# Performance work log

Hardware: AMD Instinct MI355X
Metric: run time of the kernel (lower is better)

The kernel has to match this reference:

```python
import jax, jax.numpy as jnp
import numpy as np

N_TP = 4  # number of heterogeneous agent types (experts)


def _mlp(x, w1, b1, w2, b2, w3, b3):
    h = jax.nn.relu(x @ w1 + b1)
    h = jax.nn.relu(h @ w2 + b2)
    return h @ w3 + b3


def setup_inputs() -> dict:
    key = jax.random.key(0)
    ks = jax.random.split(key, 12)
    T, A, D, H, NA = 2048, 128, 64, 64, 16
    s = 0.05
    return {
        "obs": jax.random.normal(ks[0], (T, A, D), dtype=jnp.float32),
        "hete_pick": jax.random.randint(ks[1], (T, A), 0, N_TP, dtype=jnp.int64),
        "gp_sel_summary": jax.random.uniform(ks[2], (T, N_TP), dtype=jnp.float32),
        "W1": jax.random.normal(ks[3], (N_TP, D + N_TP, H), dtype=jnp.float32) * s,
        "b1": jnp.zeros((N_TP, H), jnp.float32),
        "W2": jax.random.normal(ks[4], (N_TP, H, H), dtype=jnp.float32) * s,
        "b2": jnp.zeros((N_TP, H), jnp.float32),
        "W3": jax.random.normal(ks[5], (N_TP, H, NA), dtype=jnp.float32) * s,
        "b3": jnp.zeros((N_TP, NA), jnp.float32),
        "cW1": jax.random.normal(ks[6], (D + N_TP, H), dtype=jnp.float32) * s,
        "cb1": jnp.zeros((H,), jnp.float32),
        "cW2": jax.random.normal(ks[7], (H, H), dtype=jnp.float32) * s,
        "cb2": jnp.zeros((H,), jnp.float32),
        "cW3": jax.random.normal(ks[8], (H, 1), dtype=jnp.float32) * s,
        "cb3": jnp.zeros((1,), jnp.float32),
    }


def reference(obs, hete_pick, gp_sel_summary, W1, b1, W2, b2, W3, b3,
              cW1, cb1, cW2, cb2, cW3, cb3):
    T, A, D = obs.shape
    n_tp = W1.shape[0]
    # hete_info_obs: broadcast group-selection summary over agents, concat to obs
    hete_info = jnp.broadcast_to(gp_sel_summary[:, None, :], (T, A, n_tp))
    x = jnp.concatenate([obs, hete_info.astype(obs.dtype)], axis=-1)  # [T,A,D+n_tp]
    xf = x.reshape(T * A, D + n_tp)
    tp = hete_pick.reshape(T * A)
    # per-type dispatch: mask -> sub-net -> scatter back (expressed as masked select)
    logits = jnp.zeros((T * A, W3.shape[-1]), obs.dtype)
    for t in range(n_tp):
        out_t = _mlp(xf, W1[t], b1[t], W2[t], b2[t], W3[t], b3[t])
        logits = jnp.where((tp == t)[:, None], out_t, logits)
    # central critic runs on all agents
    value = _mlp(xf, cW1, cb1, cW2, cb2, cW3, cb3)  # [T*A,1]
    out = jnp.concatenate([logits, value], axis=-1)  # [T*A, n_action+1]
    return out.reshape(T, A, -1)
```

## Files before the change

kernel.cpp:

```cpp
#include <hip/hip_runtime.h>
#include <stdint.h>


typedef float v4f __attribute__((ext_vector_type(4)));
typedef short v8s __attribute__((ext_vector_type(8)));

#define WP2_OFF 30720
#define WP3_OFF 51200

static __device__ __forceinline__ short f2bf(float f) {
    union { float f; uint32_t u; } c; c.f = f;
    uint32_t u = c.u;
    uint32_t r = (u + 0x7FFFu + ((u >> 16) & 1u)) >> 16;
    return (short)r;
}
static __device__ __forceinline__ uint32_t pk2(float a, float b) {
    return (uint32_t)(uint16_t)f2bf(a) | ((uint32_t)(uint16_t)f2bf(b) << 16);
}

__global__ void prep_kernel(const float* __restrict__ W1, const float* __restrict__ cW1,
                            const float* __restrict__ W2, const float* __restrict__ cW2,
                            const float* __restrict__ W3, const float* __restrict__ cW3,
                            short* __restrict__ wp) {
    int b = blockIdx.x, lane = threadIdx.x;
    int nl = lane & 15, quad = lane >> 4;
    short frag[8];
    if (b < 60) {
        int e = b / 12, rem = b % 12, ks = rem / 4, nt = rem % 4;
        int n = nt * 16 + nl;
#pragma unroll
        for (int j = 0; j < 8; j++) {
            int k = ks * 32 + quad * 8 + j;
            float v = 0.f;
            if (k < 68) v = (e < 4) ? W1[(e * 68 + k) * 64 + n] : cW1[k * 64 + n];
            frag[j] = f2bf(v);
        }
    } else if (b < 100) {
        int u = b - 60, e = u / 8, ks = (u % 8) / 4, nt = u % 4;
        int n = nt * 16 + nl;
#pragma unroll
        for (int j = 0; j < 8; j++) {
            int k = ks * 32 + quad * 8 + j;
            frag[j] = f2bf((e < 4) ? W2[(e * 64 + k) * 64 + n] : cW2[k * 64 + n]);
        }
    } else {
        int u = b - 100;
#pragma unroll
        for (int j = 0; j < 8; j++) {
            int ks = (u < 8) ? (u & 1) : (u - 8);
            int k  = ks * 32 + quad * 8 + j;
            float v;
            if (u < 8) { int ee = u >> 1; v = W3[(ee * 64 + k) * 16 + nl]; }
            else       { v = (nl == 0) ? cW3[k] : 0.f; }
            frag[j] = f2bf(v);
        }
    }
    v8s pk = { frag[0], frag[1], frag[2], frag[3], frag[4], frag[5], frag[6], frag[7] };
    *(v8s*)(wp + (size_t)b * 512 + lane * 8) = pk;
}


__global__ __launch_bounds__(256, 3) void main_kernel(
    const float* __restrict__ obs, const float* __restrict__ gp,
    const int* __restrict__ hete, const short* __restrict__ wp,
    const float* __restrict__ b1, const float* __restrict__ b2, const float* __restrict__ b3,
    const float* __restrict__ cb1, const float* __restrict__ cb2, const float* __restrict__ cb3,
    float* __restrict__ out)
{
    __shared__ __align__(16) uint32_t H_[4][64 * 36];
    int tid = threadIdx.x, wv = tid >> 6, lane = tid & 63;
    int ml = lane & 15, quad = lane >> 4;
    uint32_t* H = H_[wv];
    int base = (blockIdx.x * 4 + wv) * 64;

    v8s      xf[2][4];
    uint32_t gpk[4][2];
    int      tpv[4];
    float    oE[4][4];
    float    oV[4];

#pragma unroll
    for (int tt = 0; tt < 4; tt++) {
        int tok = base + tt * 16 + ml;
        tpv[tt] = hete[tok];
        const float* xr = obs + (size_t)tok * 64 + quad * 8;
#pragma unroll
        for (int ks = 0; ks < 2; ks++) {
            float4 a = *(const float4*)(xr + ks * 32);
            float4 c = *(const float4*)(xr + ks * 32 + 4);
            v8s f;
            f[0] = f2bf(a.x); f[1] = f2bf(a.y); f[2] = f2bf(a.z); f[3] = f2bf(a.w);
            f[4] = f2bf(c.x); f[5] = f2bf(c.y); f[6] = f2bf(c.z); f[7] = f2bf(c.w);
            xf[ks][tt] = f;
        }
        if (quad == 0) {
            float4 g = *(const float4*)(gp + (size_t)(tok >> 7) * 4);
            gpk[tt][0] = pk2(g.x, g.y); gpk[tt][1] = pk2(g.z, g.w);
        } else { gpk[tt][0] = 0; gpk[tt][1] = 0; }
    }

    float cb3v = cb3[0];

    for (int ne = 0; ne < 5; ne++) {
        v4f acc[4][4];
#pragma unroll
        for (int tt = 0; tt < 4; tt++)
#pragma unroll
            for (int nt = 0; nt < 4; nt++) acc[tt][nt] = (v4f){0.f, 0.f, 0.f, 0.f};
#pragma unroll
        for (int ks = 0; ks < 3; ks++) {
            v8s wa[4];
#pragma unroll
            for (int nt = 0; nt < 4; nt++)
                wa[nt] = *(const v8s*)(wp + (size_t)((ne * 3 + ks) * 4 + nt) * 512 + lane * 8);
#pragma unroll
            for (int tt = 0; tt < 4; tt++) {
                v8s xb;
                if (ks < 2) xb = xf[ks][tt];
                else {
                    union { uint32_t u[4]; v8s s; } cv;
                    cv.u[0] = gpk[tt][0]; cv.u[1] = gpk[tt][1]; cv.u[2] = 0; cv.u[3] = 0;
                    xb = cv.s;
                }
#pragma unroll
                for (int nt = 0; nt < 4; nt++)
                    acc[tt][nt] = __builtin_amdgcn_mfma_f32_16x16x32_bf16(wa[nt], xb, acc[tt][nt], 0, 0, 0);
            }
        }
        const float* B1 = (ne < 4) ? (b1 + ne * 64) : cb1;
        float4 bv[4];
#pragma unroll
        for (int nt = 0; nt < 4; nt++) bv[nt] = *(const float4*)(B1 + nt * 16 + quad * 4);
#pragma unroll
        for (int tt = 0; tt < 4; tt++) {
            int tL = tt * 16 + ml, rb = tL * 36, sw = tL & 7;
#pragma unroll
            for (int nt = 0; nt < 4; nt++) {
                float v0 = fmaxf(acc[tt][nt][0] + bv[nt].x, 0.f);
                float v1 = fmaxf(acc[tt][nt][1] + bv[nt].y, 0.f);
                float v2 = fmaxf(acc[tt][nt][2] + bv[nt].z, 0.f);
                float v3 = fmaxf(acc[tt][nt][3] + bv[nt].w, 0.f);
                int g = 2 * nt + (quad >> 1);
                uint2 w2 = { pk2(v0, v1), pk2(v2, v3) };
                *(uint2*)&H[rb + ((g ^ sw) << 2) + 2 * (quad & 1)] = w2;
            }
        }
        v8s wa2[2][4];
#pragma unroll
        for (int ks2 = 0; ks2 < 2; ks2++)
#pragma unroll
            for (int nt = 0; nt < 4; nt++)
                wa2[ks2][nt] = *(const v8s*)(wp + WP2_OFF +
                    (size_t)((ne * 2 + ks2) * 4 + nt) * 512 + lane * 8);
        const float* B2 = (ne < 4) ? (b2 + ne * 64) : cb2;
        float4 bv2[4];
#pragma unroll
        for (int nt = 0; nt < 4; nt++) bv2[nt] = *(const float4*)(B2 + nt * 16 + quad * 4);
        v8s w3f[2];
#pragma unroll
        for (int ks2 = 0; ks2 < 2; ks2++)
            w3f[ks2] = *(const v8s*)(wp + WP3_OFF +
                (size_t)((ne < 4) ? (ne * 2 + ks2) : (8 + ks2)) * 512 + lane * 8);
        float4 b3v = (ne < 4) ? *(const float4*)(b3 + ne * 16 + quad * 4)
                              : (float4){0.f, 0.f, 0.f, 0.f};

#pragma unroll
        for (int tt = 0; tt < 4; tt++) {
            int tL = tt * 16 + ml, rb = tL * 36, sw = tL & 7;
            v4f a2[4];
#pragma unroll
            for (int nt = 0; nt < 4; nt++) a2[nt] = (v4f){0.f, 0.f, 0.f, 0.f};
#pragma unroll
            for (int ks2 = 0; ks2 < 2; ks2++) {
                v8s hf = *(const v8s*)&H[rb + (((4 * ks2 + quad) ^ sw) << 2)];
#pragma unroll
                for (int nt = 0; nt < 4; nt++)
                    a2[nt] = __builtin_amdgcn_mfma_f32_16x16x32_bf16(wa2[ks2][nt], hf, a2[nt], 0, 0, 0);
            }
#pragma unroll
            for (int nt = 0; nt < 4; nt++) {
                float v0 = fmaxf(a2[nt][0] + bv2[nt].x, 0.f);
                float v1 = fmaxf(a2[nt][1] + bv2[nt].y, 0.f);
                float v2 = fmaxf(a2[nt][2] + bv2[nt].z, 0.f);
                float v3 = fmaxf(a2[nt][3] + bv2[nt].w, 0.f);
                int g = 2 * nt + (quad >> 1);
                uint2 w2 = { pk2(v0, v1), pk2(v2, v3) };
                *(uint2*)&H[rb + ((g ^ sw) << 2) + 2 * (quad & 1)] = w2;
            }
            v4f a3 = (v4f){0.f, 0.f, 0.f, 0.f};
#pragma unroll
            for (int ks2 = 0; ks2 < 2; ks2++) {
                v8s hf2 = *(const v8s*)&H[rb + (((4 * ks2 + quad) ^ sw) << 2)];
                a3 = __builtin_amdgcn_mfma_f32_16x16x32_bf16(w3f[ks2], hf2, a3, 0, 0, 0);
            }
            if (ne < 4) {
#pragma unroll
                for (int rr = 0; rr < 4; rr++) {
                    float val = a3[rr] + ((const float*)&b3v)[rr];
                    if (tpv[tt] == ne) oE[tt][rr] = val;
                }
            } else {
                oV[tt] = a3[0] + cb3v;
            }
        }
    }

#pragma unroll
    for (int tt = 0; tt < 4; tt++) {
        int tok = base + tt * 16 + ml;
        float* o = out + (size_t)tok * 17 + quad * 4;
#pragma unroll
        for (int rr = 0; rr < 4; rr++) o[rr] = oE[tt][rr];
        if (quad == 0) out[(size_t)tok * 17 + 16] = oV[tt];
    }
}


extern "C" void kernel_launch(void* const* d_in, const int* in_sizes, int n_in,
                              void* d_out, int out_size, void* d_ws, size_t ws_size,
                              hipStream_t stream) {
    const float* obs = (const float*)d_in[0];
    const int*  hete = (const int*)d_in[1];
    const float* gp  = (const float*)d_in[2];
    const float* W1  = (const float*)d_in[3];
    const float* b1  = (const float*)d_in[4];
    const float* W2  = (const float*)d_in[5];
    const float* b2  = (const float*)d_in[6];
    const float* W3  = (const float*)d_in[7];
    const float* b3  = (const float*)d_in[8];
    const float* cW1 = (const float*)d_in[9];
    const float* cb1 = (const float*)d_in[10];
    const float* cW2 = (const float*)d_in[11];
    const float* cb2 = (const float*)d_in[12];
    const float* cW3 = (const float*)d_in[13];
    const float* cb3 = (const float*)d_in[14];
    float* out = (float*)d_out;

    short* wp = (short*)d_ws;

    prep_kernel<<<110,   64, 0, stream>>>(W1, cW1, W2, cW2, W3, cW3, wp);
    main_kernel<<<1024, 256, 0, stream>>>(obs, gp, hete, wp,
                                          b1, b2, b3, cb1, cb2, cb3, out);
}
```

Before: 192.9 us.

## Keep MLP activations in registers via permuted weight K-order, fold biases into MFMA

```diff
diff --git a/kernel.cpp b/kernel.cpp
--- a/kernel.cpp
+++ b/kernel.cpp
@@ -8,17 +8,17 @@
 #define WP2_OFF 30720
 #define WP3_OFF 51200
 
-static __device__ __forceinline__ short f2bf(float f) {
+static __device__ __forceinline__ uint32_t rna_hi(float f) {
     union { float f; uint32_t u; } c; c.f = f;
-    uint32_t u = c.u;
-    uint32_t r = (u + 0x7FFFu + ((u >> 16) & 1u)) >> 16;
-    return (short)r;
+    return (c.u + 0x8000u) >> 16;
 }
 static __device__ __forceinline__ uint32_t pk2(float a, float b) {
-    return (uint32_t)(uint16_t)f2bf(a) | ((uint32_t)(uint16_t)f2bf(b) << 16);
+    union { float f; uint32_t u; } ca, cb; ca.f = a; cb.f = b;
+    return ((ca.u + 0x8000u) >> 16) | ((cb.u + 0x8000u) & 0xffff0000u);
 }
 
 __global__ void prep_kernel(const float* __restrict__ W1, const float* __restrict__ cW1,
+                            const float* __restrict__ b1, const float* __restrict__ cb1,
                             const float* __restrict__ W2, const float* __restrict__ cW2,
                             const float* __restrict__ W3, const float* __restrict__ cW3,
                             short* __restrict__ wp) {
@@ -32,27 +32,28 @@
         for (int j = 0; j < 8; j++) {
             int k = ks * 32 + quad * 8 + j;
             float v = 0.f;
-            if (k < 68) v = (e < 4) ? W1[(e * 68 + k) * 64 + n] : cW1[k * 64 + n];
-            frag[j] = f2bf(v);
+            if (k < 68)       v = (e < 4) ? W1[(e * 68 + k) * 64 + n] : cW1[k * 64 + n];
+            else if (k == 68) v = (e < 4) ? b1[e * 64 + n] : cb1[n];
+            frag[j] = (short)rna_hi(v);
         }
     } else if (b < 100) {
         int u = b - 60, e = u / 8, ks = (u % 8) / 4, nt = u % 4;
         int n = nt * 16 + nl;
 #pragma unroll
         for (int j = 0; j < 8; j++) {
-            int k = ks * 32 + quad * 8 + j;
-            frag[j] = f2bf((e < 4) ? W2[(e * 64 + k) * 64 + n] : cW2[k * 64 + n]);
+            int ka = (2 * ks + (j >> 2)) * 16 + quad * 4 + (j & 3);
+            frag[j] = (short)rna_hi((e < 4) ? W2[(e * 64 + ka) * 64 + n] : cW2[ka * 64 + n]);
         }
     } else {
         int u = b - 100;
 #pragma unroll
         for (int j = 0; j < 8; j++) {
             int ks = (u < 8) ? (u & 1) : (u - 8);
-            int k  = ks * 32 + quad * 8 + j;
+            int ka = (2 * ks + (j >> 2)) * 16 + quad * 4 + (j & 3);
             float v;
-            if (u < 8) { int ee = u >> 1; v = W3[(ee * 64 + k) * 16 + nl]; }
-            else       { v = (nl == 0) ? cW3[k] : 0.f; }
-            frag[j] = f2bf(v);
+            if (u < 8) { int ee = u >> 1; v = W3[(ee * 64 + ka) * 16 + nl]; }
+            else       { v = (nl == 0) ? cW3[ka] : 0.f; }
+            frag[j] = (short)rna_hi(v);
         }
     }
     v8s pk = { frag[0], frag[1], frag[2], frag[3], frag[4], frag[5], frag[6], frag[7] };
@@ -60,27 +61,23 @@
 }
 
 
-__global__ __launch_bounds__(256, 3) void main_kernel(
+__global__ __launch_bounds__(256) void main_kernel(
     const float* __restrict__ obs, const float* __restrict__ gp,
     const int* __restrict__ hete, const short* __restrict__ wp,
-    const float* __restrict__ b1, const float* __restrict__ b2, const float* __restrict__ b3,
-    const float* __restrict__ cb1, const float* __restrict__ cb2, const float* __restrict__ cb3,
+    const float* __restrict__ b2, const float* __restrict__ b3,
+    const float* __restrict__ cb2, const float* __restrict__ cb3,
     float* __restrict__ out)
 {
-    __shared__ __align__(16) uint32_t H_[4][64 * 36];
     int tid = threadIdx.x, wv = tid >> 6, lane = tid & 63;
     int ml = lane & 15, quad = lane >> 4;
-    uint32_t* H = H_[wv];
-    int base = (blockIdx.x * 4 + wv) * 64;
-
-    v8s      xf[2][4];
-    uint32_t gpk[4][2];
-    int      tpv[4];
-    float    oE[4][4];
-    float    oV[4];
-
-#pragma unroll
-    for (int tt = 0; tt < 4; tt++) {
+    int base = (blockIdx.x * 4 + wv) * 32;
+
+    v8s xf[2][2];
+    v8s xg[2];
+    int tpv[2];
+
+#pragma unroll
+    for (int tt = 0; tt < 2; tt++) {
         int tok = base + tt * 16 + ml;
         tpv[tt] = hete[tok];
         const float* xr = obs + (size_t)tok * 64 + quad * 8;
@@ -88,23 +85,34 @@
         for (int ks = 0; ks < 2; ks++) {
             float4 a = *(const float4*)(xr + ks * 32);
             float4 c = *(const float4*)(xr + ks * 32 + 4);
-            v8s f;
-            f[0] = f2bf(a.x); f[1] = f2bf(a.y); f[2] = f2bf(a.z); f[3] = f2bf(a.w);
-            f[4] = f2bf(c.x); f[5] = f2bf(c.y); f[6] = f2bf(c.z); f[7] = f2bf(c.w);
-            xf[ks][tt] = f;
-        }
+            union { uint32_t u[4]; v8s s; } cv;
+            cv.u[0] = pk2(a.x, a.y); cv.u[1] = pk2(a.z, a.w);
+            cv.u[2] = pk2(c.x, c.y); cv.u[3] = pk2(c.z, c.w);
+            xf[ks][tt] = cv.s;
+        }
+        union { uint32_t u[4]; v8s s; } cg;
         if (quad == 0) {
-            float4 g = *(const float4*)(gp + (size_t)(tok >> 7) * 4);
-            gpk[tt][0] = pk2(g.x, g.y); gpk[tt][1] = pk2(g.z, g.w);
-        } else { gpk[tt][0] = 0; gpk[tt][1] = 0; }
+            float4 g = *(const float4*)(gp + (size_t)(base >> 7) * 4);
+            cg.u[0] = pk2(g.x, g.y); cg.u[1] = pk2(g.z, g.w);
+            cg.u[2] = 0x00003F80u;
+            cg.u[3] = 0;
+        } else { cg.u[0] = 0; cg.u[1] = 0; cg.u[2] = 0; cg.u[3] = 0; }
+        xg[tt] = cg.s;
     }
 
     float cb3v = cb3[0];
+    float oL[2][4];
+    float oV[2];
+#pragma unroll
+    for (int tt = 0; tt < 2; tt++) {
+        oL[tt][0] = 0.f; oL[tt][1] = 0.f; oL[tt][2] = 0.f; oL[tt][3] = 0.f;
+        oV[tt] = 0.f;
+    }
 
     for (int ne = 0; ne < 5; ne++) {
-        v4f acc[4][4];
-#pragma unroll
-        for (int tt = 0; tt < 4; tt++)
+        v4f acc[2][4];
+#pragma unroll
+        for (int tt = 0; tt < 2; tt++)
 #pragma unroll
             for (int nt = 0; nt < 4; nt++) acc[tt][nt] = (v4f){0.f, 0.f, 0.f, 0.f};
 #pragma unroll
@@ -114,35 +122,11 @@
             for (int nt = 0; nt < 4; nt++)
                 wa[nt] = *(const v8s*)(wp + (size_t)((ne * 3 + ks) * 4 + nt) * 512 + lane * 8);
 #pragma unroll
-            for (int tt = 0; tt < 4; tt++) {
-                v8s xb;
-                if (ks < 2) xb = xf[ks][tt];
-                else {
-                    union { uint32_t u[4]; v8s s; } cv;
-                    cv.u[0] = gpk[tt][0]; cv.u[1] = gpk[tt][1]; cv.u[2] = 0; cv.u[3] = 0;
-                    xb = cv.s;
-                }
+            for (int tt = 0; tt < 2; tt++) {
+                v8s xb = (ks < 2) ? xf[ks][tt] : xg[tt];
 #pragma unroll
                 for (int nt = 0; nt < 4; nt++)
                     acc[tt][nt] = __builtin_amdgcn_mfma_f32_16x16x32_bf16(wa[nt], xb, acc[tt][nt], 0, 0, 0);
-            }
-        }
-        const float* B1 = (ne < 4) ? (b1 + ne * 64) : cb1;
-        float4 bv[4];
-#pragma unroll
-        for (int nt = 0; nt < 4; nt++) bv[nt] = *(const float4*)(B1 + nt * 16 + quad * 4);
-#pragma unroll
-        for (int tt = 0; tt < 4; tt++) {
-            int tL = tt * 16 + ml, rb = tL * 36, sw = tL & 7;
-#pragma unroll
-            for (int nt = 0; nt < 4; nt++) {
-                float v0 = fmaxf(acc[tt][nt][0] + bv[nt].x, 0.f);
-                float v1 = fmaxf(acc[tt][nt][1] + bv[nt].y, 0.f);
-                float v2 = fmaxf(acc[tt][nt][2] + bv[nt].z, 0.f);
-                float v3 = fmaxf(acc[tt][nt][3] + bv[nt].w, 0.f);
-                int g = 2 * nt + (quad >> 1);
-                uint2 w2 = { pk2(v0, v1), pk2(v2, v3) };
-                *(uint2*)&H[rb + ((g ^ sw) << 2) + 2 * (quad & 1)] = w2;
             }
         }
         v8s wa2[2][4];
@@ -152,53 +136,55 @@
             for (int nt = 0; nt < 4; nt++)
                 wa2[ks2][nt] = *(const v8s*)(wp + WP2_OFF +
                     (size_t)((ne * 2 + ks2) * 4 + nt) * 512 + lane * 8);
-        const float* B2 = (ne < 4) ? (b2 + ne * 64) : cb2;
-        float4 bv2[4];
-#pragma unroll
-        for (int nt = 0; nt < 4; nt++) bv2[nt] = *(const float4*)(B2 + nt * 16 + quad * 4);
         v8s w3f[2];
 #pragma unroll
         for (int ks2 = 0; ks2 < 2; ks2++)
             w3f[ks2] = *(const v8s*)(wp + WP3_OFF +
                 (size_t)((ne < 4) ? (ne * 2 + ks2) : (8 + ks2)) * 512 + lane * 8);
-        float4 b3v = (ne < 4) ? *(const float4*)(b3 + ne * 16 + quad * 4)
-                              : (float4){0.f, 0.f, 0.f, 0.f};
-
-#pragma unroll
-        for (int tt = 0; tt < 4; tt++) {
-            int tL = tt * 16 + ml, rb = tL * 36, sw = tL & 7;
+        const float* B2 = (ne < 4) ? (b2 + ne * 64) : cb2;
+
+#pragma unroll
+        for (int tt = 0; tt < 2; tt++) {
+            v8s hf[2];
+#pragma unroll
+            for (int ks2 = 0; ks2 < 2; ks2++) {
+                union { uint32_t u[4]; v8s s; } cv;
+                cv.u[0] = pk2(fmaxf(acc[tt][2 * ks2][0], 0.f),     fmaxf(acc[tt][2 * ks2][1], 0.f));
+                cv.u[1] = pk2(fmaxf(acc[tt][2 * ks2][2], 0.f),     fmaxf(acc[tt][2 * ks2][3], 0.f));
+                cv.u[2] = pk2(fmaxf(acc[tt][2 * ks2 + 1][0], 0.f), fmaxf(acc[tt][2 * ks2 + 1][1], 0.f));
+                cv.u[3] = pk2(fmaxf(acc[tt][2 * ks2 + 1][2], 0.f), fmaxf(acc[tt][2 * ks2 + 1][3], 0.f));
+                hf[ks2] = cv.s;
+            }
             v4f a2[4];
 #pragma unroll
-            for (int nt = 0; nt < 4; nt++) a2[nt] = (v4f){0.f, 0.f, 0.f, 0.f};
+            for (int nt = 0; nt < 4; nt++)
+                a2[nt] = *(const v4f*)(B2 + nt * 16 + quad * 4);
+#pragma unroll
+            for (int ks2 = 0; ks2 < 2; ks2++)
+#pragma unroll
+                for (int nt = 0; nt < 4; nt++)
+                    a2[nt] = __builtin_amdgcn_mfma_f32_16x16x32_bf16(wa2[ks2][nt], hf[ks2], a2[nt], 0, 0, 0);
+            v8s hf2[2];
 #pragma unroll
             for (int ks2 = 0; ks2 < 2; ks2++) {
-                v8s hf = *(const v8s*)&H[rb + (((4 * ks2 + quad) ^ sw) << 2)];
-#pragma unroll
-                for (int nt = 0; nt < 4; nt++)
-                    a2[nt] = __builtin_amdgcn_mfma_f32_16x16x32_bf16(wa2[ks2][nt], hf, a2[nt], 0, 0, 0);
-            }
-#pragma unroll
-            for (int nt = 0; nt < 4; nt++) {
-                float v0 = fmaxf(a2[nt][0] + bv2[nt].x, 0.f);
-                float v1 = fmaxf(a2[nt][1] + bv2[nt].y, 0.f);
-                float v2 = fmaxf(a2[nt][2] + bv2[nt].z, 0.f);
-                float v3 = fmaxf(a2[nt][3] + bv2[nt].w, 0.f);
-                int g = 2 * nt + (quad >> 1);
-                uint2 w2 = { pk2(v0, v1), pk2(v2, v3) };
-                *(uint2*)&H[rb + ((g ^ sw) << 2) + 2 * (quad & 1)] = w2;
-            }
-            v4f a3 = (v4f){0.f, 0.f, 0.f, 0.f};
-#pragma unroll
-            for (int ks2 = 0; ks2 < 2; ks2++) {
-                v8s hf2 = *(const v8s*)&H[rb + (((4 * ks2 + quad) ^ sw) << 2)];
-                a3 = __builtin_amdgcn_mfma_f32_16x16x32_bf16(w3f[ks2], hf2, a3, 0, 0, 0);
-            }
+                union { uint32_t u[4]; v8s s; } cv;
+                cv.u[0] = pk2(fmaxf(a2[2 * ks2][0], 0.f),     fmaxf(a2[2 * ks2][1], 0.f));
+                cv.u[1] = pk2(fmaxf(a2[2 * ks2][2], 0.f),     fmaxf(a2[2 * ks2][3], 0.f));
+                cv.u[2] = pk2(fmaxf(a2[2 * ks2 + 1][0], 0.f), fmaxf(a2[2 * ks2 + 1][1], 0.f));
+                cv.u[3] = pk2(fmaxf(a2[2 * ks2 + 1][2], 0.f), fmaxf(a2[2 * ks2 + 1][3], 0.f));
+                hf2[ks2] = cv.s;
+            }
+            v4f a3;
+            if (ne < 4) a3 = *(const v4f*)(b3 + ne * 16 + quad * 4);
+            else        a3 = (v4f){0.f, 0.f, 0.f, 0.f};
+#pragma unroll
+            for (int ks2 = 0; ks2 < 2; ks2++)
+                a3 = __builtin_amdgcn_mfma_f32_16x16x32_bf16(w3f[ks2], hf2[ks2], a3, 0, 0, 0);
+
             if (ne < 4) {
 #pragma unroll
-                for (int rr = 0; rr < 4; rr++) {
-                    float val = a3[rr] + ((const float*)&b3v)[rr];
-                    if (tpv[tt] == ne) oE[tt][rr] = val;
-                }
+                for (int rr = 0; rr < 4; rr++)
+                    oL[tt][rr] = (tpv[tt] == ne) ? a3[rr] : oL[tt][rr];
             } else {
                 oV[tt] = a3[0] + cb3v;
             }
@@ -206,11 +192,13 @@
     }
 
 #pragma unroll
-    for (int tt = 0; tt < 4; tt++) {
+    for (int tt = 0; tt < 2; tt++) {
         int tok = base + tt * 16 + ml;
-        float* o = out + (size_t)tok * 17 + quad * 4;
-#pragma unroll
-        for (int rr = 0; rr < 4; rr++) o[rr] = oE[tt][rr];
+        size_t o = (size_t)tok * 17 + quad * 4;
+        out[o + 0] = oL[tt][0];
+        out[o + 1] = oL[tt][1];
+        out[o + 2] = oL[tt][2];
+        out[o + 3] = oL[tt][3];
         if (quad == 0) out[(size_t)tok * 17 + 16] = oV[tt];
     }
 }
@@ -238,7 +226,7 @@
 
     short* wp = (short*)d_ws;
 
-    prep_kernel<<<110,   64, 0, stream>>>(W1, cW1, W2, cW2, W3, cW3, wp);
-    main_kernel<<<1024, 256, 0, stream>>>(obs, gp, hete, wp,
-                                          b1, b2, b3, cb1, cb2, cb3, out);
-}
+    prep_kernel<<<110,   64, 0, stream>>>(W1, cW1, b1, cb1, W2, cW2, W3, cW3, wp);
+    main_kernel<<<2048, 256, 0, stream>>>(obs, gp, hete, wp,
+                                          b2, b3, cb2, cb3, out);
+}
```

Measured after the change: 160.8 us. -16.6%, faster.
